# Optimization experiments

Measured on AMD Instinct MI355X. Metric: run time of the kernel, lower is better.

The kernel has to match this reference:

```python
import jax, jax.numpy as jnp
import numpy as np

N_NODES = 50000
N_HYPEREDGES = 10000
N_INC = 800000  # incidences (edges in the bipartite node-hyperedge graph)
D = 128
NEG_SLOPE = 0.2


def segment_softmax(logits, seg, num_segments):
    # numerically stable softmax within segments (grouped by seg)
    m = jax.ops.segment_max(logits, seg, num_segments=num_segments)
    e = jnp.exp(logits - m[seg])
    s = jax.ops.segment_sum(e, seg, num_segments=num_segments)
    return e / s[seg]


def safe_inv(d):
    return jnp.where(d > 0, 1.0 / d, 0.0)


def setup_inputs() -> dict:
    key = jax.random.key(0)
    ks = jax.random.split(key, 8)
    x = jax.random.normal(ks[0], (N_NODES, D), dtype=jnp.float32)
    idx0 = jax.random.randint(ks[1], (N_INC,), 0, N_NODES)          # node ids
    idx1 = jax.random.randint(ks[2], (N_INC,), 0, N_HYPEREDGES)     # hyperedge ids
    hyperedge_index = jnp.stack([idx0, idx1], axis=0).astype(jnp.int64)
    hyperedge_weight = jnp.ones((N_HYPEREDGES,), dtype=jnp.float32)
    sc = 1.0 / np.sqrt(D)
    W_lin = jax.random.normal(ks[3], (D, D), dtype=jnp.float32) * sc
    W_lin2 = jax.random.normal(ks[4], (D, D), dtype=jnp.float32) * sc
    W_lin3 = jax.random.normal(ks[5], (D, D), dtype=jnp.float32) * sc
    att = jax.random.normal(ks[6], (1, 1, 2 * D), dtype=jnp.float32) * sc
    att2 = jax.random.normal(ks[7], (1, 1, 2 * D), dtype=jnp.float32) * sc
    return {"x": x, "hyperedge_index": hyperedge_index,
            "hyperedge_weight": hyperedge_weight,
            "W_lin": W_lin, "W_lin2": W_lin2, "W_lin3": W_lin3,
            "att": att, "att2": att2}


def reference(x, hyperedge_index, hyperedge_weight, W_lin, W_lin2, W_lin3, att, att2):
    N, M = N_NODES, N_HYPEREDGES
    H, F = 1, D
    idx0 = hyperedge_index[0]  # node side  [E]
    idx1 = hyperedge_index[1]  # hyperedge side [E]

    # Hyperedge(): mean-style aggregation of node features into hyperedges
    ones_e = jnp.ones_like(idx1, dtype=x.dtype)
    Binv = safe_inv(jax.ops.segment_sum(ones_e, idx1, num_segments=M))  # [M]
    he0 = jax.ops.segment_sum(x[idx0], idx1, num_segments=M) * Binv[:, None]  # [M,D]

    # linear projections
    xl = (x @ W_lin).reshape(N, H, F)      # [N,H,F]
    hl = (he0 @ W_lin2).reshape(M, H, F)   # [M,H,F]

    # first attention: node-gathered vs hyperedge-gathered, softmax grouped by node
    x_i = xl[idx0]                          # [E,H,F]
    x_j = hl[idx1]                          # [E,H,F]
    alpha = (jnp.concatenate([x_i, x_j], axis=-1) * att).sum(-1)  # [E,H]
    alpha = jax.nn.leaky_relu(alpha, NEG_SLOPE)
    alpha = segment_softmax(alpha, idx0, N)

    # degree normalizations
    Dinv = safe_inv(jax.ops.segment_sum(hyperedge_weight[idx1], idx0, num_segments=N))  # [N]

    # propagate node -> hyperedge: out_e[e] = sum Binv[e]*alpha*x[node]
    msg1 = Binv[idx1][:, None, None] * alpha[:, :, None] * x_i  # [E,H,F]
    out_e = jax.ops.segment_sum(msg1, idx1, num_segments=M)     # [M,H,F]

    # second attention with lin3-transformed hyperedge features
    he2 = (out_e.reshape(M, H * F) @ W_lin3).reshape(M, H, F)
    x_j2 = he2[idx1]
    alpha2 = (jnp.concatenate([x_i, x_j2], axis=-1) * att2).sum(-1)  # [E,H]
    alpha2 = jax.nn.leaky_relu(alpha2, NEG_SLOPE)
    alpha2 = segment_softmax(alpha2, idx0, N)

    # propagate hyperedge -> node: out_n[n] = sum Dinv[n]*alpha2*out_e[hyperedge]
    msg2 = Dinv[idx0][:, None, None] * alpha2[:, :, None] * out_e[idx1]  # [E,H,F]
    out_n = jax.ops.segment_sum(msg2, idx0, num_segments=N)              # [N,H,F]

    return out_n.reshape(N, H * F)
```

## Files before the change

kernel.cpp:

```cpp
#include <hip/hip_runtime.h>
#include <math.h>

#define DF 128
#define TILE 8192
#define CAPA 8192
#define CAPB 10240
typedef unsigned int uint;
typedef __attribute__((ext_vector_type(8))) short bf16x8;
typedef __attribute__((ext_vector_type(4))) float f32x4;

__device__ __forceinline__ float leaky(float s){ return s > 0.f ? s : 0.2f*s; }

__device__ __forceinline__ uint bfr(float f){
    uint u = __float_as_uint(f);
    return (u + 0x7fffu + ((u >> 16) & 1u)) >> 16;
}
__device__ __forceinline__ uint bf2(float a, float b){ return bfr(a) | (bfr(b) << 16); }
__device__ __forceinline__ float blo(uint v){ return __uint_as_float(v << 16); }
__device__ __forceinline__ float bhi(uint v){ return __uint_as_float(v & 0xffff0000u); }

__device__ __forceinline__ uint fenc(float f){
    uint u = __float_as_uint(f);
    return (u & 0x80000000u) ? ~u : (u | 0x80000000u);
}
__device__ __forceinline__ float fdec(uint k){
    return (k & 0x80000000u) ? __uint_as_float(k ^ 0x80000000u) : __uint_as_float(~k);
}

__device__ __forceinline__ void load_edge(const void* raw, int is64, int E, int e,
                                          int& n, int& m){
    if (is64){
        const long long* p = (const long long*)raw;
        n = (int)p[e]; m = (int)p[(long long)E + e];
    } else {
        const int* p = (const int*)raw;
        n = p[e]; m = p[E + e];
    }
}

__global__ __launch_bounds__(256) void prep(
        const uint* __restrict__ raw, int* __restrict__ ctrl,
        int* __restrict__ gcurA, int* __restrict__ gcurB,
        const float* __restrict__ W1, const float* __restrict__ W2,
        const float* __restrict__ W3,
        const float* __restrict__ att, const float* __restrict__ att2,
        float* __restrict__ w2a, float* __restrict__ v1,
        float* __restrict__ v2, float* __restrict__ v3,
        uint* __restrict__ W1t, int E)
{
    int t = threadIdx.x;
    int bid = blockIdx.x;
    if (bid == 0){
        __shared__ int cnt;
        gcurA[t] = t*CAPA;
        gcurB[t] = t*CAPB;
        if (t == 0){ cnt = 0; ctrl[1] = 0; ctrl[2] = 0; }
        __syncthreads();
        int nz = 0;
        for (int i = 0; i < 4; i++){
            int w = 2*(t*4 + i) + 1;
            if (w < 2*E) nz += (raw[w] != 0u);
        }
        atomicAdd(&cnt, nz);
        __syncthreads();
        if (t == 0) ctrl[0] = (cnt == 0) ? 1 : 0;
    } else if (bid == 1){
        int d = t & 127;
        const float* W = (t < 128) ? W2 : W1;
        const float* a = (t < 128) ? (att + 128) : att;
        float s = 0.f;
        for (int f = 0; f < 128; f++) s += W[d*128 + f]*a[f];
        if (t < 128) w2a[d] = s; else v1[d] = s;
    } else if (bid == 2){
        __shared__ float sw3a[128];
        int d = t & 127;
        const float* W = (t < 128) ? W1 : W3;
        const float* a = (t < 128) ? att2 : (att2 + 128);
        float s = 0.f;
        for (int f = 0; f < 128; f++) s += W[d*128 + f]*a[f];
        if (t < 128) v2[d] = s; else sw3a[d] = s;
        __syncthreads();
        if (t < 128){
            float s2 = 0.f;
            for (int f = 0; f < 128; f++) s2 += W1[t*128 + f]*sw3a[f];
            v3[t] = s2;
        }
    } else {
        int base = (bid - 3)*1024;
        for (int p = base + t; p < base + 1024; p += 256){
            int f = p >> 6, dh = p & 63;
            W1t[p] = bf2(W1[(2*dh)*128 + f], W1[(2*dh + 1)*128 + f]);
        }
    }
}

__global__ __launch_bounds__(512) void scatter_gemm(
        const void* __restrict__ raw, const int* __restrict__ ctrl,
        int* __restrict__ gcurA, int* __restrict__ gcurB,
        uint* __restrict__ bktA, uint* __restrict__ bktB,
        const float* __restrict__ X, const uint* __restrict__ W1t,
        const float* __restrict__ w2a, const float* __restrict__ v1,
        const float* __restrict__ v2, const float* __restrict__ v3,
        uint* __restrict__ xlb, float* __restrict__ a1x, float* __restrict__ a2x,
        float* __restrict__ px, float* __restrict__ pxl,
        int E, int N, int SC)
{
    __shared__ char smem[73728];
    int t = threadIdx.x;
    int bid = blockIdx.x;

    if (bid < SC){
        uint* stA = (uint*)smem;
        uint* stB = (uint*)(smem + 32768);
        int*  hA  = (int*)(smem + 65536);
        int*  scA = hA + 256; int* cuA = hA + 512; int* bA = hA + 768;
        int*  hB  = hA + 1024; int* scB = hA + 1280; int* cuB = hA + 1536; int* bB = hA + 1792;
        if (t < 256){ hA[t] = 0; hB[t] = 0; }
        __syncthreads();
        int tb = bid*TILE;
        int cnt = min(TILE, E - tb);
        int is64 = ctrl[0];
        for (int i = t; i < cnt; i += 512){
            int n, m; load_edge(raw, is64, E, tb + i, n, m);
            atomicAdd(&hA[n >> 8], 1);
            atomicAdd(&hB[m >> 6], 1);
        }
        __syncthreads();
        if (t < 256){ scA[t] = hA[t]; scB[t] = hB[t]; }
        __syncthreads();
        for (int off = 1; off < 256; off <<= 1){
            int vA = 0, vB = 0;
            if (t < 256 && t >= off){ vA = scA[t - off]; vB = scB[t - off]; }
            __syncthreads();
            if (t < 256){ scA[t] += vA; scB[t] += vB; }
            __syncthreads();
        }
        if (t < 256){
            scA[t] -= hA[t]; scB[t] -= hB[t];
            cuA[t] = scA[t]; cuB[t] = scB[t];
            bA[t] = atomicAdd(&gcurA[t], hA[t]);
            bB[t] = atomicAdd(&gcurB[t], hB[t]);
        }
        __syncthreads();
        for (int i = t; i < cnt; i += 512){
            int n, m; load_edge(raw, is64, E, tb + i, n, m);
            int pA = atomicAdd(&cuA[n >> 8], 1);
            stA[pA] = ((uint)n << 14) | (uint)m;
            int pB = atomicAdd(&cuB[m >> 6], 1);
            stB[pB] = ((uint)m << 16) | (uint)n;
        }
        __syncthreads();
        for (int p = t; p < cnt; p += 512){
            uint v = stA[p]; int b = (int)(v >> 22);
            bktA[bA[b] + (p - scA[b])] = v;
            uint w = stB[p]; int c = (int)(w >> 22);
            bktB[bB[c] + (p - scB[c])] = w;
        }
    } else {
        char* lds = smem;
        int lane = t & 63, wv = t >> 6;
        int row0 = (bid - SC)*128;
        {
            const uint4* g = (const uint4*)W1t;
            #pragma unroll
            for (int i = 0; i < 4; i++){
                int u = i*512 + t;
                int col = u >> 4;
                uint4 v = g[u];
                *(uint4*)(lds + 32768 + ((u*16) ^ ((col & 7) << 4))) = v;
            }
        }
        {
            int cg = t & 31;
            float4 c_px = ((const float4*)w2a)[cg];
            float4 c_a1 = ((const float4*)v1 )[cg];
            float4 c_a2 = ((const float4*)v2 )[cg];
            float4 c_pl = ((const float4*)v3 )[cg];
            #pragma unroll
            for (int i = 0; i < 8; i++){
                int idx = i*512 + t;
                int rl = idx >> 5;
                int row = row0 + rl;
                float4 xv = make_float4(0.f, 0.f, 0.f, 0.f);
                if (row < N) xv = ((const float4*)X)[(size_t)row*32 + cg];
                uint2 pk; pk.x = bf2(xv.x, xv.y); pk.y = bf2(xv.z, xv.w);
                *(uint2*)(lds + rl*256 + ((cg*8) ^ ((rl & 7) << 4))) = pk;
                float d0 = xv.x*c_px.x + xv.y*c_px.y + xv.z*c_px.z + xv.w*c_px.w;
                float d1 = xv.x*c_a1.x + xv.y*c_a1.y + xv.z*c_a1.z + xv.w*c_a1.w;
                float d2 = xv.x*c_a2.x + xv.y*c_a2.y + xv.z*c_a2.z + xv.w*c_a2.w;
                float d3 = xv.x*c_pl.x + xv.y*c_pl.y + xv.z*c_pl.z + xv.w*c_pl.w;
                #pragma unroll
                for (int off = 16; off > 0; off >>= 1){
                    d0 += __shfl_xor(d0, off); d1 += __shfl_xor(d1, off);
                    d2 += __shfl_xor(d2, off); d3 += __shfl_xor(d3, off);
                }
                if (cg == 0 && row < N){
                    px[row] = d0; a1x[row] = d1; a2x[row] = d2; pxl[row] = d3;
                }
            }
        }
        __syncthreads();
        f32x4 acc[8];
        #pragma unroll
        for (int i = 0; i < 8; i++) acc[i] = (f32x4){0.f, 0.f, 0.f, 0.f};
        int arow = wv*16 + (lane & 15);
        int aswz = (arow & 7) << 4;
        int bswz = (lane & 7) << 4;
        #pragma unroll
        for (int ks = 0; ks < 4; ks++){
            int au16 = ((lane >> 4) + ks*4)*16;
            bf16x8 af = *(const bf16x8*)(lds + arow*256 + (au16 ^ aswz));
            #pragma unroll
            for (int nf = 0; nf < 8; nf++){
                int bcol = nf*16 + (lane & 15);
                bf16x8 bf = *(const bf16x8*)(lds + 32768 + bcol*256 + (au16 ^ bswz));
                acc[nf] = __builtin_amdgcn_mfma_f32_16x16x32_bf16(af, bf, acc[nf], 0, 0, 0);
            }
        }
        __syncthreads();
        #pragma unroll
        for (int nf = 0; nf < 8; nf++){
            #pragma unroll
            for (int reg = 0; reg < 4; reg++){
                int rl = wv*16 + (lane >> 4)*4 + reg;
                int col = nf*16 + (lane & 15);
                *(unsigned short*)(lds + rl*256 + ((col*2) ^ ((rl & 7) << 4))) =
                    (unsigned short)bfr(acc[nf][reg]);
            }
        }
        __syncthreads();
        #pragma unroll
        for (int j = 0; j < 4; j++){
            int unit = j*64 + lane;
            int rl = wv*16 + (unit >> 4);
            int uu = unit & 15;
            uint4 v = *(const uint4*)(lds + rl*256 + ((uu*16) ^ ((rl & 7) << 4)));
            int grow = row0 + rl;
            if (grow < N) ((uint4*)xlb)[(size_t)grow*16 + uu] = v;
        }
    }
}

__global__ __launch_bounds__(256) void csr_edge(
        const uint* __restrict__ bktB, const int* __restrict__ gcurB,
        int* __restrict__ adj1, int2* __restrict__ rg1,
        const float* __restrict__ px, float* __restrict__ a1h,
        uint* __restrict__ g1key, int M)
{
    __shared__ int h[64], sc[64], cu[64];
    __shared__ float fsum[64];
    int t = threadIdx.x;
    int b = blockIdx.x;
    int sb = b*CAPB;
    int total = gcurB[b] - sb;
    int kb = b << 6;
    if (t < 64){ h[t] = 0; fsum[t] = 0.f; }
    __syncthreads();
    const uint* src = bktB + sb;
    for (int i = t; i < total; i += 256)
        atomicAdd(&h[(int)(src[i] >> 16) - kb], 1);
    __syncthreads();
    if (t < 64) sc[t] = h[t];
    __syncthreads();
    for (int off = 1; off < 64; off <<= 1){
        int v = (t < 64 && t >= off) ? sc[t - off] : 0;
        __syncthreads();
        if (t < 64) sc[t] += v;
        __syncthreads();
    }
    if (t < 64){ sc[t] -= h[t]; cu[t] = sc[t]; }
    __syncthreads();
    for (int i = t; i < total; i += 256){
        uint v = src[i];
        int k = (int)(v >> 16) - kb;
        int pos = atomicAdd(&cu[k], 1);
        int n = (int)(v & 0xFFFFu);
        adj1[sb + pos] = n;
        atomicAdd(&fsum[k], px[n]);
    }
    __syncthreads();
    if (t < 64){
        int key = kb + t;
        float av = -3.4e38f;
        if (key < M){
            av = (h[t] > 0) ? fsum[t]/(float)h[t] : 0.f;
            rg1[key] = make_int2(sb + sc[t], sb + sc[t] + h[t]);
            a1h[key] = av;
        }
        #pragma unroll
        for (int off = 32; off > 0; off >>= 1)
            av = fmaxf(av, __shfl_xor(av, off));
        if (t == 0) atomicMax(g1key, fenc(av));
    }
}

__global__ __launch_bounds__(256) void csr_node(
        const uint* __restrict__ bktA, const int* __restrict__ gcurA,
        int* __restrict__ adj0, int2* __restrict__ rg0,
        const float* __restrict__ a1x, const float* __restrict__ a1h,
        const float* __restrict__ hw, const float* __restrict__ pxl,
        const uint* __restrict__ g1key, uint* __restrict__ g2key,
        float4* __restrict__ pk1, float* __restrict__ Dinv, int N)
{
    __shared__ int h[256], sc[256], cu[256];
    __shared__ uint sm[CAPA];
    __shared__ float wmax[4];
    int t = threadIdx.x;
    int b = blockIdx.x;
    int sb = b*CAPA;
    int total = gcurA[b] - sb;
    int kb = b << 8;
    float G1 = fdec(*g1key);
    h[t] = 0;
    __syncthreads();
    const uint* src = bktA + sb;
    for (int i = t; i < total; i += 256)
        atomicAdd(&h[(int)(src[i] >> 14) - kb], 1);
    __syncthreads();
    sc[t] = h[t];
    __syncthreads();
    for (int off = 1; off < 256; off <<= 1){
        int v = (t >= off) ? sc[t - off] : 0;
        __syncthreads();
        sc[t] += v;
        __syncthreads();
    }
    sc[t] -= h[t];
    cu[t] = sc[t];
    __syncthreads();
    for (int i = t; i < total; i += 256){
        uint v = src[i];
        int k = (int)(v >> 14) - kb;
        int pos = atomicAdd(&cu[k], 1);
        sm[pos] = v & 0x3FFFu;
    }
    __syncthreads();
    for (int i = t; i < total; i += 256) adj0[sb + i] = (int)sm[i];
    int key = kb + t;
    float pl = (key < N) ? pxl[key] : 0.f;
    if (key < N){
        int deg = h[t], beg = sc[t];
        rg0[key] = make_int2(sb + beg, sb + beg + deg);
        float ax = a1x[key];
        float mx = leaky(ax + G1);
        float se = 0.f, wsum = 0.f;
        for (int j = 0; j < deg; j++){
            int m = (int)sm[beg + j];
            wsum += hw[m];
            se += expf(leaky(ax + a1h[m]) - mx);
        }
        pk1[key] = make_float4(ax, mx, (deg > 0) ? 1.f/se : 0.f, pl);
        Dinv[key] = (wsum > 0.f) ? 1.f/wsum : 0.f;
    }
    float pv = pl;
    #pragma unroll
    for (int off = 32; off > 0; off >>= 1) pv = fmaxf(pv, __shfl_xor(pv, off));
    if ((t & 63) == 0) wmax[t >> 6] = pv;
    __syncthreads();
    if (t == 0){
        float bm = fmaxf(fmaxf(wmax[0], wmax[1]), fmaxf(wmax[2], wmax[3]));
        atomicMax(g2key, fenc(fmaxf(bm, 0.f)));
    }
}

__global__ __launch_bounds__(256) void agg_oute(
    const int2* __restrict__ rg1, const int* __restrict__ adj1,
    const float4* __restrict__ pk1, const float* __restrict__ a1h,
    const uint* __restrict__ xlb, uint* __restrict__ outeb,
    float* __restrict__ a2h, int M)
{
    int m = blockIdx.x*4 + (threadIdx.x >> 6);
    int lane = threadIdx.x & 63;
    if (m >= M) return;
    int2 r = rg1[m];
    int b = r.x, e = r.y, deg = e - b;
    float binv = deg > 0 ? 1.f/(float)deg : 0.f;
    float ah = a1h[m];
    int sub = lane >> 4, cg = lane & 15;
    const uint4* x4p = (const uint4*)xlb;
    float acc[8] = {0,0,0,0,0,0,0,0};
    float sca = 0.f;
    for (int base = b; base < e; base += 64){
        int cnt = min(64, e - base);
        int n = 0; float al = 0.f;
        if (lane < cnt){
            n = adj1[base + lane];
            float4 g = pk1[n];
            al = expf(leaky(g.x + ah) - g.y) * g.z;
            sca += al * g.w;
        }
        int t4 = 0;
        for (; t4 + 8 <= cnt; t4 += 8){
            int   nb0 = __shfl(n,  t4 + sub);
            float ab0 = __shfl(al, t4 + sub);
            int   nb1 = __shfl(n,  t4 + 4 + sub);
            float ab1 = __shfl(al, t4 + 4 + sub);
            uint4 v0 = x4p[(size_t)nb0*16 + cg];
            uint4 v1 = x4p[(size_t)nb1*16 + cg];
            acc[0] += ab0*blo(v0.x); acc[1] += ab0*bhi(v0.x);
            acc[2] += ab0*blo(v0.y); acc[3] += ab0*bhi(v0.y);
            acc[4] += ab0*blo(v0.z); acc[5] += ab0*bhi(v0.z);
            acc[6] += ab0*blo(v0.w); acc[7] += ab0*bhi(v0.w);
            acc[0] += ab1*blo(v1.x); acc[1] += ab1*bhi(v1.x);
            acc[2] += ab1*blo(v1.y); acc[3] += ab1*bhi(v1.y);
            acc[4] += ab1*blo(v1.z); acc[5] += ab1*bhi(v1.z);
            acc[6] += ab1*blo(v1.w); acc[7] += ab1*bhi(v1.w);
        }
        for (; t4 < cnt; t4 += 4){
            int   nb = __shfl(n,  t4 + sub);
            float ab = __shfl(al, t4 + sub);
            uint4 v = x4p[(size_t)nb*16 + cg];
            acc[0] += ab*blo(v.x); acc[1] += ab*bhi(v.x);
            acc[2] += ab*blo(v.y); acc[3] += ab*bhi(v.y);
            acc[4] += ab*blo(v.z); acc[5] += ab*bhi(v.z);
            acc[6] += ab*blo(v.w); acc[7] += ab*bhi(v.w);
        }
    }
    #pragma unroll
    for (int i = 0; i < 8; i++){
        acc[i] += __shfl_xor(acc[i], 32);
        acc[i] += __shfl_xor(acc[i], 16);
    }
    #pragma unroll
    for (int off = 32; off > 0; off >>= 1) sca += __shfl_xor(sca, off);
    if (lane < 16){
        uint4 w;
        w.x = bf2(binv*acc[0], binv*acc[1]);
        w.y = bf2(binv*acc[2], binv*acc[3]);
        w.z = bf2(binv*acc[4], binv*acc[5]);
        w.w = bf2(binv*acc[6], binv*acc[7]);
        ((uint4*)outeb)[(size_t)m*16 + cg] = w;
    }
    if (lane == 0) a2h[m] = binv*sca;
}

__global__ __launch_bounds__(256) void agg_outn(
    const int2* __restrict__ rg0, const int* __restrict__ adj0,
    const float* __restrict__ a2x, const float* __restrict__ a2h,
    const float* __restrict__ Dinv, const uint* __restrict__ outeb,
    const uint* __restrict__ g2key, float* __restrict__ out, int N)
{
    int n = blockIdx.x*4 + (threadIdx.x >> 6);
    int lane = threadIdx.x & 63;
    if (n >= N) return;
    int2 r = rg0[n];
    int b = r.x, e = r.y;
    float ax = a2x[n];
    float mx = leaky(ax + fdec(*g2key));
    int sub = lane >> 4, cg = lane & 15;
    const uint4* o4p = (const uint4*)outeb;
    float acc[8] = {0,0,0,0,0,0,0,0};
    float sa = 0.f;
    for (int base = b; base < e; base += 64){
        int cnt = min(64, e - base);
        int m = 0; float al = 0.f;
        if (lane < cnt){
            m = adj0[base + lane];
            al = expf(leaky(ax + a2h[m]) - mx);
            sa += al;
        }
        int t4 = 0;
        for (; t4 + 8 <= cnt; t4 += 8){
            int   mb0 = __shfl(m,  t4 + sub);
            float ab0 = __shfl(al, t4 + sub);
            int   mb1 = __shfl(m,  t4 + 4 + sub);
            float ab1 = __shfl(al, t4 + 4 + sub);
            uint4 v0 = o4p[(size_t)mb0*16 + cg];
            uint4 v1 = o4p[(size_t)mb1*16 + cg];
            acc[0] += ab0*blo(v0.x); acc[1] += ab0*bhi(v0.x);
            acc[2] += ab0*blo(v0.y); acc[3] += ab0*bhi(v0.y);
            acc[4] += ab0*blo(v0.z); acc[5] += ab0*bhi(v0.z);
            acc[6] += ab0*blo(v0.w); acc[7] += ab0*bhi(v0.w);
            acc[0] += ab1*blo(v1.x); acc[1] += ab1*bhi(v1.x);
            acc[2] += ab1*blo(v1.y); acc[3] += ab1*bhi(v1.y);
            acc[4] += ab1*blo(v1.z); acc[5] += ab1*bhi(v1.z);
            acc[6] += ab1*blo(v1.w); acc[7] += ab1*bhi(v1.w);
        }
        for (; t4 < cnt; t4 += 4){
            int   mb = __shfl(m,  t4 + sub);
            float ab = __shfl(al, t4 + sub);
            uint4 v = o4p[(size_t)mb*16 + cg];
            acc[0] += ab*blo(v.x); acc[1] += ab*bhi(v.x);
            acc[2] += ab*blo(v.y); acc[3] += ab*bhi(v.y);
            acc[4] += ab*blo(v.z); acc[5] += ab*bhi(v.z);
            acc[6] += ab*blo(v.w); acc[7] += ab*bhi(v.w);
        }
    }
    #pragma unroll
    for (int off = 32; off > 0; off >>= 1) sa += __shfl_xor(sa, off);
    #pragma unroll
    for (int i = 0; i < 8; i++){
        acc[i] += __shfl_xor(acc[i], 32);
        acc[i] += __shfl_xor(acc[i], 16);
    }
    float scale = (sa > 0.f) ? Dinv[n]/sa : 0.f;
    if (lane < 16){
        float4 o0 = make_float4(scale*acc[0], scale*acc[1], scale*acc[2], scale*acc[3]);
        float4 o1 = make_float4(scale*acc[4], scale*acc[5], scale*acc[6], scale*acc[7]);
        ((float4*)out)[(size_t)n*32 + cg*2]     = o0;
        ((float4*)out)[(size_t)n*32 + cg*2 + 1] = o1;
    }
}

extern "C" void kernel_launch(void* const* d_in, const int* in_sizes, int n_in,
                              void* d_out, int out_size, void* d_ws, size_t ws_size,
                              hipStream_t stream){
    const float* x    = (const float*)d_in[0];
    const void*  hidx = d_in[1];
    const float* hw   = (const float*)d_in[2];
    const float* W1   = (const float*)d_in[3];
    const float* W2   = (const float*)d_in[4];
    const float* W3   = (const float*)d_in[5];
    const float* att  = (const float*)d_in[6];
    const float* att2 = (const float*)d_in[7];
    float* out = (float*)d_out;

    const int N = in_sizes[0] / DF;
    const int E = in_sizes[1] / 2;
    const int M = in_sizes[2];

    char* ws = (char*)d_ws;
    size_t o = 0;
    auto take = [&](size_t bytes) -> char* {
        char* p = ws + o;
        o += (bytes + 255) & ~(size_t)255;
        return p;
    };
    const int nbA = (N + 255) >> 8;
    const int nbB = (M + 63) >> 6;

    uint*   xlb  = (uint*)  take((size_t)N*64*4);
    uint*   outeb= (uint*)  take((size_t)M*64*4);
    float*  a1x  = (float*) take((size_t)N*4);
    float*  a2x  = (float*) take((size_t)N*4);
    float*  px   = (float*) take((size_t)N*4);
    float*  pxl  = (float*) take((size_t)N*4);
    float*  Dinv = (float*) take((size_t)N*4);
    float*  a1h  = (float*) take((size_t)M*4);
    float*  a2h  = (float*) take((size_t)M*4);
    float4* pk1  = (float4*)take((size_t)N*16);
    float*  w2a  = (float*) take(DF*4);
    float*  v1   = (float*) take(DF*4);
    float*  v2   = (float*) take(DF*4);
    float*  v3   = (float*) take(DF*4);
    uint*   W1t  = (uint*)  take(128*64*4);
    int2*   rg0  = (int2*)  take((size_t)N*8);
    int2*   rg1  = (int2*)  take((size_t)M*8);
    int*    gcurA= (int*)   take(256*4);
    int*    gcurB= (int*)   take(256*4);
    uint*   bktA = (uint*)  take((size_t)nbA*CAPA*4 + TILE*4);
    uint*   bktB = (uint*)  take((size_t)nbB*CAPB*4 + TILE*4);
    int*    adj0 = (int*)   take((size_t)nbA*CAPA*4);
    int*    adj1 = (int*)   take((size_t)nbB*CAPB*4);
    int*    ctrl = (int*)   take(256);

    const int SC = (E + TILE - 1)/TILE;
    const int GB = (N + 127)/128;

    prep<<<11, 256, 0, stream>>>((const uint*)hidx, ctrl, gcurA, gcurB,
                                 W1, W2, W3, att, att2, w2a, v1, v2, v3, W1t, E);
    scatter_gemm<<<SC + GB, 512, 0, stream>>>(hidx, ctrl, gcurA, gcurB,
                                 bktA, bktB, x, W1t, w2a, v1, v2, v3,
                                 xlb, a1x, a2x, px, pxl, E, N, SC);
    csr_edge<<<nbB, 256, 0, stream>>>(bktB, gcurB, adj1, rg1, px, a1h,
                                      (uint*)&ctrl[1], M);
    csr_node<<<nbA, 256, 0, stream>>>(bktA, gcurA, adj0, rg0,
                                      a1x, a1h, hw, pxl, (uint*)&ctrl[1],
                                      (uint*)&ctrl[2], pk1, Dinv, N);
    agg_oute<<<(M + 3)/4, 256, 0, stream>>>(rg1, adj1, pk1, a1h, xlb, outeb,
                                            a2h, M);
    agg_outn<<<(N + 3)/4, 256, 0, stream>>>(rg0, adj0, a2x, a2h, Dinv, outeb,
                                            (uint*)&ctrl[2], out, N);
}
```

Before: 124.9 us.

## Merge CSR kernels with ticket-based inter-block wait and cache edges in LDS

Fuses the hyperedge-side and node-side CSR build kernels into one launch. Node blocks do their sort and bucketing first, then spin on a global ticket until every hyperedge block has published a1h and the global max, and only then compute the softmax denominators. The scatter phase also halves its tile size and keeps the packed edges in LDS so the second pass does not reload them from global memory. This removes one kernel launch and lets the two CSR phases overlap, but the spin-wait can deadlock if the node blocks are resident while hyperedge blocks cannot be scheduled.

```diff
diff --git a/kernel.cpp b/kernel.cpp
--- a/kernel.cpp
+++ b/kernel.cpp
@@ -2,7 +2,7 @@
 #include <math.h>
 
 #define DF 128
-#define TILE 8192
+#define TILE 4096
 #define CAPA 8192
 #define CAPB 10240
 typedef unsigned int uint;
@@ -54,7 +54,7 @@
         __shared__ int cnt;
         gcurA[t] = t*CAPA;
         gcurB[t] = t*CAPB;
-        if (t == 0){ cnt = 0; ctrl[1] = 0; ctrl[2] = 0; }
+        if (t == 0){ cnt = 0; ctrl[1] = 0; ctrl[2] = 0; ctrl[3] = 0; }
         __syncthreads();
         int nz = 0;
         for (int i = 0; i < 4; i++){
@@ -110,9 +110,10 @@
     int bid = blockIdx.x;
 
     if (bid < SC){
-        uint* stA = (uint*)smem;
-        uint* stB = (uint*)(smem + 32768);
-        int*  hA  = (int*)(smem + 65536);
+        uint* edges = (uint*)smem;
+        uint* stA   = (uint*)(smem + 16384);
+        uint* stB   = (uint*)(smem + 32768);
+        int*  hA  = (int*)(smem + 49152);
         int*  scA = hA + 256; int* cuA = hA + 512; int* bA = hA + 768;
         int*  hB  = hA + 1024; int* scB = hA + 1280; int* cuB = hA + 1536; int* bB = hA + 1792;
         if (t < 256){ hA[t] = 0; hB[t] = 0; }
@@ -122,6 +123,8 @@
         int is64 = ctrl[0];
         for (int i = t; i < cnt; i += 512){
             int n, m; load_edge(raw, is64, E, tb + i, n, m);
+            uint v = ((uint)n << 14) | (uint)m;
+            edges[i] = v;
             atomicAdd(&hA[n >> 8], 1);
             atomicAdd(&hB[m >> 6], 1);
         }
@@ -143,9 +146,10 @@
         }
         __syncthreads();
         for (int i = t; i < cnt; i += 512){
-            int n, m; load_edge(raw, is64, E, tb + i, n, m);
+            uint v = edges[i];
+            int n = (int)(v >> 14), m = (int)(v & 0x3FFFu);
             int pA = atomicAdd(&cuA[n >> 8], 1);
-            stA[pA] = ((uint)n << 14) | (uint)m;
+            stA[pA] = v;
             int pB = atomicAdd(&cuB[m >> 6], 1);
             stB[pB] = ((uint)m << 16) | (uint)n;
         }
@@ -241,125 +245,131 @@
     }
 }
 
-__global__ __launch_bounds__(256) void csr_edge(
+__global__ __launch_bounds__(256) void csr_both(
         const uint* __restrict__ bktB, const int* __restrict__ gcurB,
         int* __restrict__ adj1, int2* __restrict__ rg1,
         const float* __restrict__ px, float* __restrict__ a1h,
-        uint* __restrict__ g1key, int M)
-{
-    __shared__ int h[64], sc[64], cu[64];
-    __shared__ float fsum[64];
-    int t = threadIdx.x;
-    int b = blockIdx.x;
-    int sb = b*CAPB;
-    int total = gcurB[b] - sb;
-    int kb = b << 6;
-    if (t < 64){ h[t] = 0; fsum[t] = 0.f; }
-    __syncthreads();
-    const uint* src = bktB + sb;
-    for (int i = t; i < total; i += 256)
-        atomicAdd(&h[(int)(src[i] >> 16) - kb], 1);
-    __syncthreads();
-    if (t < 64) sc[t] = h[t];
-    __syncthreads();
-    for (int off = 1; off < 64; off <<= 1){
-        int v = (t < 64 && t >= off) ? sc[t - off] : 0;
-        __syncthreads();
-        if (t < 64) sc[t] += v;
-        __syncthreads();
-    }
-    if (t < 64){ sc[t] -= h[t]; cu[t] = sc[t]; }
-    __syncthreads();
-    for (int i = t; i < total; i += 256){
-        uint v = src[i];
-        int k = (int)(v >> 16) - kb;
-        int pos = atomicAdd(&cu[k], 1);
-        int n = (int)(v & 0xFFFFu);
-        adj1[sb + pos] = n;
-        atomicAdd(&fsum[k], px[n]);
-    }
-    __syncthreads();
-    if (t < 64){
-        int key = kb + t;
-        float av = -3.4e38f;
-        if (key < M){
-            av = (h[t] > 0) ? fsum[t]/(float)h[t] : 0.f;
-            rg1[key] = make_int2(sb + sc[t], sb + sc[t] + h[t]);
-            a1h[key] = av;
-        }
-        #pragma unroll
-        for (int off = 32; off > 0; off >>= 1)
-            av = fmaxf(av, __shfl_xor(av, off));
-        if (t == 0) atomicMax(g1key, fenc(av));
-    }
-}
-
-__global__ __launch_bounds__(256) void csr_node(
+        uint* __restrict__ g1key,
         const uint* __restrict__ bktA, const int* __restrict__ gcurA,
         int* __restrict__ adj0, int2* __restrict__ rg0,
-        const float* __restrict__ a1x, const float* __restrict__ a1h,
-        const float* __restrict__ hw, const float* __restrict__ pxl,
-        const uint* __restrict__ g1key, uint* __restrict__ g2key,
-        float4* __restrict__ pk1, float* __restrict__ Dinv, int N)
+        const float* __restrict__ a1x, const float* __restrict__ hw,
+        const float* __restrict__ pxl, uint* __restrict__ g2key,
+        float4* __restrict__ pk1, float* __restrict__ Dinv,
+        int* __restrict__ ticket, int N, int M, int nbB)
 {
     __shared__ int h[256], sc[256], cu[256];
     __shared__ uint sm[CAPA];
+    __shared__ float fsum[64];
     __shared__ float wmax[4];
     int t = threadIdx.x;
-    int b = blockIdx.x;
-    int sb = b*CAPA;
-    int total = gcurA[b] - sb;
-    int kb = b << 8;
-    float G1 = fdec(*g1key);
-    h[t] = 0;
-    __syncthreads();
-    const uint* src = bktA + sb;
-    for (int i = t; i < total; i += 256)
-        atomicAdd(&h[(int)(src[i] >> 14) - kb], 1);
-    __syncthreads();
-    sc[t] = h[t];
-    __syncthreads();
-    for (int off = 1; off < 256; off <<= 1){
-        int v = (t >= off) ? sc[t - off] : 0;
-        __syncthreads();
-        sc[t] += v;
-        __syncthreads();
-    }
-    sc[t] -= h[t];
-    cu[t] = sc[t];
-    __syncthreads();
-    for (int i = t; i < total; i += 256){
-        uint v = src[i];
-        int k = (int)(v >> 14) - kb;
-        int pos = atomicAdd(&cu[k], 1);
-        sm[pos] = v & 0x3FFFu;
-    }
-    __syncthreads();
-    for (int i = t; i < total; i += 256) adj0[sb + i] = (int)sm[i];
-    int key = kb + t;
-    float pl = (key < N) ? pxl[key] : 0.f;
-    if (key < N){
+
+    if (blockIdx.x < nbB){
+        int b = blockIdx.x;
+        int sb = b*CAPB;
+        int total = gcurB[b] - sb;
+        int kb = b << 6;
+        if (t < 64){ h[t] = 0; fsum[t] = 0.f; }
+        __syncthreads();
+        const uint* src = bktB + sb;
+        for (int i = t; i < total; i += 256)
+            atomicAdd(&h[(int)(src[i] >> 16) - kb], 1);
+        __syncthreads();
+        if (t < 64) sc[t] = h[t];
+        __syncthreads();
+        for (int off = 1; off < 64; off <<= 1){
+            int v = (t < 64 && t >= off) ? sc[t - off] : 0;
+            __syncthreads();
+            if (t < 64) sc[t] += v;
+            __syncthreads();
+        }
+        if (t < 64){ sc[t] -= h[t]; cu[t] = sc[t]; }
+        __syncthreads();
+        for (int i = t; i < total; i += 256){
+            uint v = src[i];
+            int k = (int)(v >> 16) - kb;
+            int pos = atomicAdd(&cu[k], 1);
+            int n = (int)(v & 0xFFFFu);
+            adj1[sb + pos] = n;
+            atomicAdd(&fsum[k], px[n]);
+        }
+        __syncthreads();
+        if (t < 64){
+            int key = kb + t;
+            float av = -3.4e38f;
+            if (key < M){
+                av = (h[t] > 0) ? fsum[t]/(float)h[t] : 0.f;
+                rg1[key] = make_int2(sb + sc[t], sb + sc[t] + h[t]);
+                a1h[key] = av;
+            }
+            #pragma unroll
+            for (int off = 32; off > 0; off >>= 1)
+                av = fmaxf(av, __shfl_xor(av, off));
+            if (t == 0) atomicMax(g1key, fenc(av));
+        }
+        __threadfence();
+        __syncthreads();
+        if (t == 0) atomicAdd(ticket, 1);
+    } else {
+        int b = blockIdx.x - nbB;
+        int sb = b*CAPA;
+        int total = gcurA[b] - sb;
+        int kb = b << 8;
+        h[t] = 0;
+        __syncthreads();
+        const uint* src = bktA + sb;
+        for (int i = t; i < total; i += 256)
+            atomicAdd(&h[(int)(src[i] >> 14) - kb], 1);
+        __syncthreads();
+        sc[t] = h[t];
+        __syncthreads();
+        for (int off = 1; off < 256; off <<= 1){
+            int v = (t >= off) ? sc[t - off] : 0;
+            __syncthreads();
+            sc[t] += v;
+            __syncthreads();
+        }
+        sc[t] -= h[t];
+        cu[t] = sc[t];
+        __syncthreads();
+        for (int i = t; i < total; i += 256){
+            uint v = src[i];
+            int k = (int)(v >> 14) - kb;
+            int pos = atomicAdd(&cu[k], 1);
+            sm[pos] = v & 0x3FFFu;
+        }
+        __syncthreads();
+        for (int i = t; i < total; i += 256) adj0[sb + i] = (int)sm[i];
+        int key = kb + t;
         int deg = h[t], beg = sc[t];
-        rg0[key] = make_int2(sb + beg, sb + beg + deg);
-        float ax = a1x[key];
-        float mx = leaky(ax + G1);
-        float se = 0.f, wsum = 0.f;
-        for (int j = 0; j < deg; j++){
-            int m = (int)sm[beg + j];
-            wsum += hw[m];
-            se += expf(leaky(ax + a1h[m]) - mx);
-        }
-        pk1[key] = make_float4(ax, mx, (deg > 0) ? 1.f/se : 0.f, pl);
-        Dinv[key] = (wsum > 0.f) ? 1.f/wsum : 0.f;
-    }
-    float pv = pl;
-    #pragma unroll
-    for (int off = 32; off > 0; off >>= 1) pv = fmaxf(pv, __shfl_xor(pv, off));
-    if ((t & 63) == 0) wmax[t >> 6] = pv;
-    __syncthreads();
-    if (t == 0){
-        float bm = fmaxf(fmaxf(wmax[0], wmax[1]), fmaxf(wmax[2], wmax[3]));
-        atomicMax(g2key, fenc(fmaxf(bm, 0.f)));
+        if (key < N) rg0[key] = make_int2(sb + beg, sb + beg + deg);
+        float pl = (key < N) ? pxl[key] : 0.f;
+        float pv = pl;
+        #pragma unroll
+        for (int off = 32; off > 0; off >>= 1) pv = fmaxf(pv, __shfl_xor(pv, off));
+        if ((t & 63) == 0) wmax[t >> 6] = pv;
+        __syncthreads();
+        if (t == 0){
+            float bm = fmaxf(fmaxf(wmax[0], wmax[1]), fmaxf(wmax[2], wmax[3]));
+            atomicMax(g2key, fenc(fmaxf(bm, 0.f)));
+        }
+        if (t == 0){
+            while (atomicAdd(ticket, 0) < nbB) __builtin_amdgcn_s_sleep(2);
+        }
+        __syncthreads();
+        __threadfence();
+        float G1 = fdec((uint)atomicAdd((int*)g1key, 0));
+        if (key < N){
+            float ax = a1x[key];
+            float mx = leaky(ax + G1);
+            float se = 0.f, wsum = 0.f;
+            for (int j = 0; j < deg; j++){
+                int m = (int)sm[beg + j];
+                wsum += hw[m];
+                se += expf(leaky(ax + a1h[m]) - mx);
+            }
+            pk1[key] = make_float4(ax, mx, (deg > 0) ? 1.f/se : 0.f, pl);
+            Dinv[key] = (wsum > 0.f) ? 1.f/wsum : 0.f;
+        }
     }
 }
 
@@ -562,11 +572,11 @@
     scatter_gemm<<<SC + GB, 512, 0, stream>>>(hidx, ctrl, gcurA, gcurB,
                                  bktA, bktB, x, W1t, w2a, v1, v2, v3,
                                  xlb, a1x, a2x, px, pxl, E, N, SC);
-    csr_edge<<<nbB, 256, 0, stream>>>(bktB, gcurB, adj1, rg1, px, a1h,
-                                      (uint*)&ctrl[1], M);
-    csr_node<<<nbA, 256, 0, stream>>>(bktA, gcurA, adj0, rg0,
-                                      a1x, a1h, hw, pxl, (uint*)&ctrl[1],
-                                      (uint*)&ctrl[2], pk1, Dinv, N);
+    csr_both<<<nbB + nbA, 256, 0, stream>>>(bktB, gcurB, adj1, rg1, px, a1h,
+                                 (uint*)&ctrl[1],
+                                 bktA, gcurA, adj0, rg0, a1x, hw, pxl,
+                                 (uint*)&ctrl[2], pk1, Dinv, &ctrl[3],
+                                 N, M, nbB);
     agg_oute<<<(M + 3)/4, 256, 0, stream>>>(rg1, adj1, pk1, a1h, xlb, outeb,
                                             a2h, M);
     agg_outn<<<(N + 3)/4, 256, 0, stream>>>(rg0, adj0, a2x, a2h, Dinv, outeb,
```

Result: slower. 176.8 us (+41.6%).
